# Optimization experiments

Measured on AMD Instinct MI355X. Metric: run time of the kernel, lower is better.

Reference implementation:

```python
import jax, jax.numpy as jnp
import numpy as np

N, E = 50000, 800000
IN, HID, HEADS, EDIM, OUT = 128, 32, 4, 16, 1
W = HID * HEADS  # 128, encoder width


def _glorot(key, shape):
    fan_in = shape[0]
    return jax.random.normal(key, shape, dtype=jnp.float32) / np.sqrt(fan_in)


def setup_inputs() -> dict:
    key = jax.random.key(0)
    ks = jax.random.split(key, 24)
    inp = {
        "x": jax.random.normal(ks[0], (N, IN), dtype=jnp.float32),
        "edge_index": jax.random.randint(ks[1], (2, E), 0, N, dtype=jnp.int64),
        "edge_attr": jax.random.normal(ks[2], (E, EDIM), dtype=jnp.float32),
        # layer 0 (in_channels -> heads*hidden)
        "Wl0": _glorot(ks[3], (IN, W)), "bl0": jnp.zeros((W,), jnp.float32),
        "Wr0": _glorot(ks[4], (IN, W)), "br0": jnp.zeros((W,), jnp.float32),
        "We0": _glorot(ks[5], (EDIM, W)),
        "att0": _glorot(ks[6], (HEADS, HID)),
        "b0": jnp.zeros((W,), jnp.float32),
        # layer 1 (heads*hidden -> heads*hidden)
        "Wl1": _glorot(ks[7], (W, W)), "bl1": jnp.zeros((W,), jnp.float32),
        "Wr1": _glorot(ks[8], (W, W)), "br1": jnp.zeros((W,), jnp.float32),
        "We1": _glorot(ks[9], (EDIM, W)),
        "att1": _glorot(ks[10], (HEADS, HID)),
        "b1": jnp.zeros((W,), jnp.float32),
        # classifier
        "Wc": _glorot(ks[11], (W, OUT)), "bc": jnp.zeros((OUT,), jnp.float32),
    }
    return inp


def _gatv2_layer(x, src, dst, ea, Wl, bl, Wr, br, We, att, b, n_nodes):
    # GATv2Conv (PyG defaults: share_weights=False, negative_slope=0.2, concat=True)
    H, C = att.shape
    xl = (x @ Wl + bl).reshape(n_nodes, H, C)   # source-side transform
    xr = (x @ Wr + br).reshape(n_nodes, H, C)   # target-side transform
    eh = (ea @ We).reshape(-1, H, C)            # edge feature transform (no bias)
    m = xl[src] + xr[dst] + eh                  # [E', H, C] per-edge message pre-activation
    e = jnp.einsum('ehc,hc->eh', jax.nn.leaky_relu(m, 0.2), att)  # [E', H]
    # segment softmax over incoming edges of each dst node (self-loops ensure no empty segment)
    emax = jax.ops.segment_max(e, dst, num_segments=n_nodes)
    ex = jnp.exp(e - emax[dst])
    denom = jax.ops.segment_sum(ex, dst, num_segments=n_nodes)
    alpha = ex / (denom[dst] + 1e-16)
    out = jax.ops.segment_sum(alpha[..., None] * xl[src], dst, num_segments=n_nodes)
    return out.reshape(n_nodes, H * C) + b


def reference(x, edge_index, edge_attr,
              Wl0, bl0, Wr0, br0, We0, att0, b0,
              Wl1, bl1, Wr1, br1, We1, att1, b1,
              Wc, bc):
    n = x.shape[0]
    src, dst = edge_index[0], edge_index[1]
    # add_self_loops with fill_value='mean': self-loop edge_attr = mean of incoming edge_attr per node
    cnt = jax.ops.segment_sum(jnp.ones((src.shape[0],), x.dtype), dst, num_segments=n)
    loop_attr = jax.ops.segment_sum(edge_attr, dst, num_segments=n) / jnp.maximum(cnt, 1.0)[:, None]
    loop = jnp.arange(n, dtype=src.dtype)
    src_a = jnp.concatenate([src, loop])
    dst_a = jnp.concatenate([dst, loop])
    ea_a = jnp.concatenate([edge_attr, loop_attr], axis=0)

    h = jax.nn.gelu(_gatv2_layer(x, src_a, dst_a, ea_a, Wl0, bl0, Wr0, br0, We0, att0, b0, n), approximate=False)
    h = jax.nn.gelu(_gatv2_layer(h, src_a, dst_a, ea_a, Wl1, bl1, Wr1, br1, We1, att1, b1, n), approximate=False)
    logits = h @ Wc + bc  # [N, 1]  (dropout inactive in eval mode)
    return logits.squeeze(-1)
```

## Files before the change

### kernel.cpp

```cpp
#include <hip/hip_runtime.h>
#include <math.h>


static inline size_t align256(size_t x) { return (x + 255) & ~size_t(255); }

__device__ __forceinline__ int clampi(int v, int lo, int hi) {
  return v < lo ? lo : (v > hi ? hi : v);
}

__global__ void k_hist(const int* __restrict__ ei, int* __restrict__ cnt, int E, int n) {
  int i = blockIdx.x * blockDim.x + threadIdx.x;
  if (i >= E) return;
  int dst = clampi(ei[E + i], 0, n - 1);
  atomicAdd(&cnt[dst], 1);
}

__global__ void k_scan(const int* __restrict__ cnt, int* __restrict__ row_ptr, int n) {
  const int T = 1024;
  __shared__ int wsum[16], wbase[16];
  int tid = threadIdx.x;
  int chunk = (n + T - 1) / T;
  int lo = tid * chunk; if (lo > n) lo = n;
  int hi = lo + chunk;  if (hi > n) hi = n;
  int s = 0;
  for (int i = lo; i < hi; ++i) s += cnt[i] + 1;
  int lane = tid & 63, w = tid >> 6;
  int incl = s;
  #pragma unroll
  for (int d = 1; d < 64; d <<= 1) {
    int v = __shfl_up(incl, d, 64);
    if (lane >= d) incl += v;
  }
  if (lane == 63) wsum[w] = incl;
  __syncthreads();
  if (tid == 0) {
    int a = 0;
    for (int i = 0; i < 16; ++i) { wbase[i] = a; a += wsum[i]; }
  }
  __syncthreads();
  int run = wbase[w] + (incl - s);
  if (tid == 0) row_ptr[0] = 0;
  for (int i = lo; i < hi; ++i) { run += cnt[i] + 1; row_ptr[i + 1] = run; }
}

__global__ void k_scatter(const int* __restrict__ ei, int* __restrict__ cursor,
                          int2* __restrict__ col, int E, int n) {
  int i = blockIdx.x * blockDim.x + threadIdx.x;
  if (i < E) {
    int src = clampi(ei[i], 0, n - 1);
    int dst = clampi(ei[E + i], 0, n - 1);
    int pos = atomicAdd(&cursor[dst], 1);
    col[pos] = make_int2(src, i);
  } else if (i < E + n) {
    int node = i - E;
    int pos = atomicAdd(&cursor[node], 1);
    col[pos] = make_int2(node, E + node);
  }
}

__global__ void k_loop_mean(const int* __restrict__ row_ptr, const int2* __restrict__ col,
                            const float* __restrict__ ea, float* __restrict__ lsum,
                            int n, int E) {
  int t = blockIdx.x * blockDim.x + threadIdx.x;
  if (t >= n * 16) return;
  int node = t >> 4, d = t & 15;
  int beg = row_ptr[node], end = row_ptr[node + 1];
  float s = 0.f;
  int c = 0;
  for (int i = beg; i < end; ++i) {
    int2 se = col[i];
    if (se.y < E) { s += ea[(size_t)se.y * 16 + d]; ++c; }
  }
  lsum[t] = s / (float)(c > 0 ? c : 1);
}

__launch_bounds__(256)
__global__ void k_transform(const float* __restrict__ in, const float* __restrict__ Wl,
                            const float* __restrict__ bl, const float* __restrict__ Wr,
                            const float* __restrict__ br, float* __restrict__ xl,
                            float* __restrict__ xr, int n) {
  __shared__ float As[16][128];
  int tid = threadIdx.x;
  int row0 = blockIdx.x * 16;
  int rows = n - row0; if (rows > 16) rows = 16;
  const float4* in4 = (const float4*)(in + (size_t)row0 * 128);
  float4* As4 = (float4*)As;
  for (int i = tid; i < rows * 32; i += 256) As4[i] = in4[i];
  __syncthreads();
  int c = tid;
  const float* B = (c < 128) ? Wl : Wr;
  int cc = c & 127;
  float bias = (c < 128) ? bl[cc] : br[cc];
  float acc[16];
  #pragma unroll
  for (int i = 0; i < 16; ++i) acc[i] = bias;
  for (int k = 0; k < 128; k += 4) {
    float b0 = B[(k + 0) * 128 + cc], b1 = B[(k + 1) * 128 + cc];
    float b2 = B[(k + 2) * 128 + cc], b3 = B[(k + 3) * 128 + cc];
    #pragma unroll
    for (int r = 0; r < 16; ++r) {
      float4 a = *(const float4*)&As[r][k];
      acc[r] += a.x * b0 + a.y * b1 + a.z * b2 + a.w * b3;
    }
  }
  float* op = (c < 128) ? xl : xr;
  for (int r = 0; r < rows; ++r) op[(size_t)(row0 + r) * 128 + cc] = acc[r];
}

#define EDGE_STEP(SRC, EID, MX, DEN, A0, A1)                                     \
  do {                                                                           \
    const float* ep = ((EID) < E) ? (ea + (size_t)(EID) * 16)                    \
                                  : (loop_attr + (size_t)((EID) - E) * 16);      \
    float2 xlv = *(const float2*)(xl + (size_t)(SRC) * 128 + lane * 2);          \
    float4 v0 = ((const float4*)ep)[0];                                          \
    float4 v1 = ((const float4*)ep)[1];                                          \
    float4 v2 = ((const float4*)ep)[2];                                          \
    float4 v3 = ((const float4*)ep)[3];                                          \
    float eh0 = v0.x * we0[0] + v0.y * we0[1] + v0.z * we0[2] + v0.w * we0[3];   \
    float eh1 = v0.x * we1[0] + v0.y * we1[1] + v0.z * we1[2] + v0.w * we1[3];   \
    eh0 += v1.x * we0[4] + v1.y * we0[5] + v1.z * we0[6] + v1.w * we0[7];        \
    eh1 += v1.x * we1[4] + v1.y * we1[5] + v1.z * we1[6] + v1.w * we1[7];        \
    eh0 += v2.x * we0[8] + v2.y * we0[9] + v2.z * we0[10] + v2.w * we0[11];      \
    eh1 += v2.x * we1[8] + v2.y * we1[9] + v2.z * we1[10] + v2.w * we1[11];      \
    eh0 += v3.x * we0[12] + v3.y * we0[13] + v3.z * we0[14] + v3.w * we0[15];    \
    eh1 += v3.x * we1[12] + v3.y * we1[13] + v3.z * we1[14] + v3.w * we1[15];    \
    float m0 = xlv.x + xrv.x + eh0;                                              \
    float m1 = xlv.y + xrv.y + eh1;                                              \
    float l0 = fmaxf(m0, 0.2f * m0);                        \
    float l1 = fmaxf(m1, 0.2f * m1);                                             \
    float p = l0 * att0 + l1 * att1;                                             \
    p += __shfl_xor(p, 1);                                                       \
    p += __shfl_xor(p, 2);                                                       \
    p += __shfl_xor(p, 4);                                                       \
    p += __shfl_xor(p, 8);                                                       \
    float nm = fmaxf(MX, p);                                                     \
    float sc = __expf(MX - nm);                                                  \
    float w  = __expf(p - nm);                                                   \
    DEN = DEN * sc + w;                                                          \
    A0  = A0 * sc + w * xlv.x;                                                   \
    A1  = A1 * sc + w * xlv.y;                                                   \
    MX  = nm;                                                                    \
  } while (0)

__launch_bounds__(256)
__global__ void k_aggregate(const float* __restrict__ xl, const float* __restrict__ xr,
                            const int* __restrict__ row_ptr, const int2* __restrict__ col,
                            const float* __restrict__ ea, const float* __restrict__ loop_attr,
                            const float* __restrict__ We, const float* __restrict__ att,
                            const float* __restrict__ bvec, float* __restrict__ out,
                            int n, int E) {
  int wv = threadIdx.x >> 6, lane = threadIdx.x & 63;
  int node = blockIdx.x * 4 + wv;
  if (node >= n) return;
  int c0 = lane * 2, c1 = lane * 2 + 1;
  float we0[16], we1[16];
  #pragma unroll
  for (int d = 0; d < 16; ++d) {
    we0[d] = We[d * 128 + c0];
    we1[d] = We[d * 128 + c1];
  }
  float att0 = att[c0], att1 = att[c1];
  float2 xrv = *(const float2*)(xr + (size_t)node * 128 + lane * 2);
  int beg = __builtin_amdgcn_readfirstlane(row_ptr[node]);
  int end = __builtin_amdgcn_readfirstlane(row_ptr[node + 1]);
  float mA = -INFINITY, dA = 0.f, a0A = 0.f, a1A = 0.f;
  float mB = -INFINITY, dB = 0.f, a0B = 0.f, a1B = 0.f;
  int i = beg;
  #pragma unroll 2
  for (; i + 1 < end; i += 2) {
    int2 sa = col[i];
    int2 sb = col[i + 1];
    int srcA = __builtin_amdgcn_readfirstlane(sa.x);
    int eidA = __builtin_amdgcn_readfirstlane(sa.y);
    int srcB = __builtin_amdgcn_readfirstlane(sb.x);
    int eidB = __builtin_amdgcn_readfirstlane(sb.y);
    EDGE_STEP(srcA, eidA, mA, dA, a0A, a1A);
    EDGE_STEP(srcB, eidB, mB, dB, a0B, a1B);
  }
  if (i < end) {
    int2 sa = col[i];
    int srcA = __builtin_amdgcn_readfirstlane(sa.x);
    int eidA = __builtin_amdgcn_readfirstlane(sa.y);
    EDGE_STEP(srcA, eidA, mA, dA, a0A, a1A);
  }
  float nm = fmaxf(mA, mB);
  float eA = __expf(mA - nm), eB = __expf(mB - nm);
  float den  = dA * eA + dB * eB;
  float acc0 = a0A * eA + a0B * eB;
  float acc1 = a1A * eA + a1B * eB;
  float inv = 1.f / (den + 1e-16f);
  float2 bv = ((const float2*)bvec)[lane];
  float o0 = acc0 * inv + bv.x;
  float o1 = acc1 * inv + bv.y;
  o0 = 0.5f * o0 * (1.f + erff(o0 * 0.70710678118654752f));
  o1 = 0.5f * o1 * (1.f + erff(o1 * 0.70710678118654752f));
  *(float2*)(out + (size_t)node * 128 + lane * 2) = make_float2(o0, o1);
}

__global__ void k_classifier(const float* __restrict__ h, const float* __restrict__ Wc,
                             const float* __restrict__ bc, float* __restrict__ out, int n) {
  int node = blockIdx.x * blockDim.x + threadIdx.x;
  if (node >= n) return;
  const float4* hp = (const float4*)(h + (size_t)node * 128);
  const float4* wp = (const float4*)Wc;
  float acc = 0.f;
  #pragma unroll
  for (int k = 0; k < 32; ++k) {
    float4 a = hp[k];
    float4 w = wp[k];
    acc += a.x * w.x + a.y * w.y + a.z * w.z + a.w * w.w;
  }
  out[node] = acc + bc[0];
}

extern "C" void kernel_launch(void* const* d_in, const int* in_sizes, int n_in,
                              void* d_out, int out_size, void* d_ws, size_t ws_size,
                              hipStream_t stream) {
  const float* x    = (const float*)d_in[0];
  const int*   ei   = (const int*)d_in[1];
  const float* ea   = (const float*)d_in[2];
  const float* Wl0  = (const float*)d_in[3];
  const float* bl0  = (const float*)d_in[4];
  const float* Wr0  = (const float*)d_in[5];
  const float* br0  = (const float*)d_in[6];
  const float* We0  = (const float*)d_in[7];
  const float* att0 = (const float*)d_in[8];
  const float* b0   = (const float*)d_in[9];
  const float* Wl1  = (const float*)d_in[10];
  const float* bl1  = (const float*)d_in[11];
  const float* Wr1  = (const float*)d_in[12];
  const float* br1  = (const float*)d_in[13];
  const float* We1  = (const float*)d_in[14];
  const float* att1 = (const float*)d_in[15];
  const float* b1   = (const float*)d_in[16];
  const float* Wc   = (const float*)d_in[17];
  const float* bc   = (const float*)d_in[18];
  float* out = (float*)d_out;

  int n  = in_sizes[0] / 128;
  int E  = in_sizes[1] / 2;
  int Ep = E + n;

  char* ws = (char*)d_ws;
  size_t off = 0;
  auto alloc = [&](size_t bytes) { size_t o = off; off = align256(off + bytes); return o; };
  int*   cnt     = (int*)  (ws + alloc((size_t)n * 4));
  float* lsum    = (float*)(ws + alloc((size_t)n * 16 * 4));
  int*   row_ptr = (int*)  (ws + alloc((size_t)(n + 1) * 4));
  int*   cursor  = (int*)  (ws + alloc((size_t)n * 4));
  int2*  col     = (int2*) (ws + alloc((size_t)Ep * 8));
  float* xl      = (float*)(ws + alloc((size_t)n * 128 * 4));
  float* xr      = (float*)(ws + alloc((size_t)n * 128 * 4));
  float* hbuf    = (float*)(ws + alloc((size_t)n * 128 * 4));
  (void)ws_size; (void)n_in; (void)out_size;

  hipMemsetAsync(cnt, 0, (size_t)n * 4, stream);
  k_hist<<<(E + 255) / 256, 256, 0, stream>>>(ei, cnt, E, n);
  k_scan<<<1, 1024, 0, stream>>>(cnt, row_ptr, n);
  hipMemcpyAsync(cursor, row_ptr, (size_t)n * 4, hipMemcpyDeviceToDevice, stream);
  k_scatter<<<(Ep + 255) / 256, 256, 0, stream>>>(ei, cursor, col, E, n);
  k_loop_mean<<<(n * 16 + 255) / 256, 256, 0, stream>>>(row_ptr, col, ea, lsum, n, E);

  k_transform<<<(n + 15) / 16, 256, 0, stream>>>(x, Wl0, bl0, Wr0, br0, xl, xr, n);
  k_aggregate<<<(n + 3) / 4, 256, 0, stream>>>(xl, xr, row_ptr, col, ea, lsum,
                                               We0, att0, b0, hbuf, n, E);
  k_transform<<<(n + 15) / 16, 256, 0, stream>>>(hbuf, Wl1, bl1, Wr1, br1, xl, xr, n);
  k_aggregate<<<(n + 3) / 4, 256, 0, stream>>>(xl, xr, row_ptr, col, ea, lsum,
                                               We1, att1, b1, hbuf, n, E);
  k_classifier<<<(n + 255) / 256, 256, 0, stream>>>(hbuf, Wc, bc, out, n);
}
```

Before: 821.0 us.

## Fuse classifier into final aggregate, widen edge unroll, drop LDS in transform

The final aggregate kernel now computes the classifier dot product with a wave-wide shuffle reduction and writes logits directly. This removes the classifier launch and the write and re-read of the final hidden buffer. The aggregate loop now keeps four independent online-softmax accumulators instead of two, giving more memory-level parallelism across edges. The transform kernel handles 32 rows per block and reads activations straight from global memory (broadcast float4 loads) instead of staging them in LDS, at the cost of more registers and uncached-in-LDS reads.

```diff
diff --git a/kernel.cpp b/kernel.cpp
--- a/kernel.cpp
+++ b/kernel.cpp
@@ -74,36 +74,43 @@
   lsum[t] = s / (float)(c > 0 ? c : 1);
 }
 
+#define TR_ROWS 32
 __launch_bounds__(256)
 __global__ void k_transform(const float* __restrict__ in, const float* __restrict__ Wl,
                             const float* __restrict__ bl, const float* __restrict__ Wr,
                             const float* __restrict__ br, float* __restrict__ xl,
                             float* __restrict__ xr, int n) {
-  __shared__ float As[16][128];
   int tid = threadIdx.x;
-  int row0 = blockIdx.x * 16;
-  int rows = n - row0; if (rows > 16) rows = 16;
-  const float4* in4 = (const float4*)(in + (size_t)row0 * 128);
-  float4* As4 = (float4*)As;
-  for (int i = tid; i < rows * 32; i += 256) As4[i] = in4[i];
-  __syncthreads();
-  int c = tid;
-  const float* B = (c < 128) ? Wl : Wr;
-  int cc = c & 127;
-  float bias = (c < 128) ? bl[cc] : br[cc];
-  float acc[16];
+  int row0 = blockIdx.x * TR_ROWS;
+  int rows = n - row0; if (rows > TR_ROWS) rows = TR_ROWS;
+  int cc = tid & 127;
+  const float* B = (tid < 128) ? Wl : Wr;
+  float bias = (tid < 128) ? bl[cc] : br[cc];
+  float acc[TR_ROWS];
   #pragma unroll
-  for (int i = 0; i < 16; ++i) acc[i] = bias;
-  for (int k = 0; k < 128; k += 4) {
-    float b0 = B[(k + 0) * 128 + cc], b1 = B[(k + 1) * 128 + cc];
-    float b2 = B[(k + 2) * 128 + cc], b3 = B[(k + 3) * 128 + cc];
-    #pragma unroll
-    for (int r = 0; r < 16; ++r) {
-      float4 a = *(const float4*)&As[r][k];
-      acc[r] += a.x * b0 + a.y * b1 + a.z * b2 + a.w * b3;
+  for (int r = 0; r < TR_ROWS; ++r) acc[r] = bias;
+  const float* Ab = in + (size_t)row0 * 128;
+  if (rows == TR_ROWS) {
+    for (int k = 0; k < 128; k += 4) {
+      float b0 = B[(k + 0) * 128 + cc], b1 = B[(k + 1) * 128 + cc];
+      float b2 = B[(k + 2) * 128 + cc], b3 = B[(k + 3) * 128 + cc];
+      #pragma unroll
+      for (int r = 0; r < TR_ROWS; ++r) {
+        float4 a = *(const float4*)(Ab + r * 128 + k);
+        acc[r] += a.x * b0 + a.y * b1 + a.z * b2 + a.w * b3;
+      }
     }
-  }
-  float* op = (c < 128) ? xl : xr;
+  } else {
+    for (int k = 0; k < 128; k += 4) {
+      float b0 = B[(k + 0) * 128 + cc], b1 = B[(k + 1) * 128 + cc];
+      float b2 = B[(k + 2) * 128 + cc], b3 = B[(k + 3) * 128 + cc];
+      for (int r = 0; r < rows; ++r) {
+        float4 a = *(const float4*)(Ab + r * 128 + k);
+        acc[r] += a.x * b0 + a.y * b1 + a.z * b2 + a.w * b3;
+      }
+    }
+  }
+  float* op = (tid < 128) ? xl : xr;
   for (int r = 0; r < rows; ++r) op[(size_t)(row0 + r) * 128 + cc] = acc[r];
 }
 
@@ -147,7 +154,8 @@
                             const int* __restrict__ row_ptr, const int2* __restrict__ col,
                             const float* __restrict__ ea, const float* __restrict__ loop_attr,
                             const float* __restrict__ We, const float* __restrict__ att,
-                            const float* __restrict__ bvec, float* __restrict__ out,
+                            const float* __restrict__ bvec, float* __restrict__ outv,
+                            const float* __restrict__ Wc, const float* __restrict__ bc,
                             int n, int E) {
   int wv = threadIdx.x >> 6, lane = threadIdx.x & 63;
   int node = blockIdx.x * 4 + wv;
@@ -165,52 +173,54 @@
   int end = __builtin_amdgcn_readfirstlane(row_ptr[node + 1]);
   float mA = -INFINITY, dA = 0.f, a0A = 0.f, a1A = 0.f;
   float mB = -INFINITY, dB = 0.f, a0B = 0.f, a1B = 0.f;
+  float mC = -INFINITY, dC = 0.f, a0C = 0.f, a1C = 0.f;
+  float mD = -INFINITY, dD = 0.f, a0D = 0.f, a1D = 0.f;
   int i = beg;
-  #pragma unroll 2
-  for (; i + 1 < end; i += 2) {
-    int2 sa = col[i];
-    int2 sb = col[i + 1];
-    int srcA = __builtin_amdgcn_readfirstlane(sa.x);
-    int eidA = __builtin_amdgcn_readfirstlane(sa.y);
-    int srcB = __builtin_amdgcn_readfirstlane(sb.x);
-    int eidB = __builtin_amdgcn_readfirstlane(sb.y);
+  for (; i + 3 < end; i += 4) {
+    int2 s0 = col[i], s1 = col[i + 1], s2 = col[i + 2], s3 = col[i + 3];
+    int srcA = __builtin_amdgcn_readfirstlane(s0.x);
+    int eidA = __builtin_amdgcn_readfirstlane(s0.y);
+    int srcB = __builtin_amdgcn_readfirstlane(s1.x);
+    int eidB = __builtin_amdgcn_readfirstlane(s1.y);
+    int srcC = __builtin_amdgcn_readfirstlane(s2.x);
+    int eidC = __builtin_amdgcn_readfirstlane(s2.y);
+    int srcD = __builtin_amdgcn_readfirstlane(s3.x);
+    int eidD = __builtin_amdgcn_readfirstlane(s3.y);
     EDGE_STEP(srcA, eidA, mA, dA, a0A, a1A);
     EDGE_STEP(srcB, eidB, mB, dB, a0B, a1B);
-  }
-  if (i < end) {
-    int2 sa = col[i];
-    int srcA = __builtin_amdgcn_readfirstlane(sa.x);
-    int eidA = __builtin_amdgcn_readfirstlane(sa.y);
+    EDGE_STEP(srcC, eidC, mC, dC, a0C, a1C);
+    EDGE_STEP(srcD, eidD, mD, dD, a0D, a1D);
+  }
+  for (; i < end; ++i) {
+    int2 s0 = col[i];
+    int srcA = __builtin_amdgcn_readfirstlane(s0.x);
+    int eidA = __builtin_amdgcn_readfirstlane(s0.y);
     EDGE_STEP(srcA, eidA, mA, dA, a0A, a1A);
   }
-  float nm = fmaxf(mA, mB);
+  float nm = fmaxf(fmaxf(mA, mB), fmaxf(mC, mD));
   float eA = __expf(mA - nm), eB = __expf(mB - nm);
-  float den  = dA * eA + dB * eB;
-  float acc0 = a0A * eA + a0B * eB;
-  float acc1 = a1A * eA + a1B * eB;
+  float eC = __expf(mC - nm), eD = __expf(mD - nm);
+  float den  = dA * eA + dB * eB + dC * eC + dD * eD;
+  float acc0 = a0A * eA + a0B * eB + a0C * eC + a0D * eD;
+  float acc1 = a1A * eA + a1B * eB + a1C * eC + a1D * eD;
   float inv = 1.f / (den + 1e-16f);
   float2 bv = ((const float2*)bvec)[lane];
   float o0 = acc0 * inv + bv.x;
   float o1 = acc1 * inv + bv.y;
   o0 = 0.5f * o0 * (1.f + erff(o0 * 0.70710678118654752f));
   o1 = 0.5f * o1 * (1.f + erff(o1 * 0.70710678118654752f));
-  *(float2*)(out + (size_t)node * 128 + lane * 2) = make_float2(o0, o1);
-}
-
-__global__ void k_classifier(const float* __restrict__ h, const float* __restrict__ Wc,
-                             const float* __restrict__ bc, float* __restrict__ out, int n) {
-  int node = blockIdx.x * blockDim.x + threadIdx.x;
-  if (node >= n) return;
-  const float4* hp = (const float4*)(h + (size_t)node * 128);
-  const float4* wp = (const float4*)Wc;
-  float acc = 0.f;
-  #pragma unroll
-  for (int k = 0; k < 32; ++k) {
-    float4 a = hp[k];
-    float4 w = wp[k];
-    acc += a.x * w.x + a.y * w.y + a.z * w.z + a.w * w.w;
-  }
-  out[node] = acc + bc[0];
+  if (Wc) {
+    float part = o0 * Wc[c0] + o1 * Wc[c1];
+    part += __shfl_xor(part, 1);
+    part += __shfl_xor(part, 2);
+    part += __shfl_xor(part, 4);
+    part += __shfl_xor(part, 8);
+    part += __shfl_xor(part, 16);
+    part += __shfl_xor(part, 32);
+    if (lane == 0) outv[node] = part + bc[0];
+  } else {
+    *(float2*)(outv + (size_t)node * 128 + lane * 2) = make_float2(o0, o1);
+  }
 }
 
 extern "C" void kernel_launch(void* const* d_in, const int* in_sizes, int n_in,
@@ -261,11 +271,10 @@
   k_scatter<<<(Ep + 255) / 256, 256, 0, stream>>>(ei, cursor, col, E, n);
   k_loop_mean<<<(n * 16 + 255) / 256, 256, 0, stream>>>(row_ptr, col, ea, lsum, n, E);
 
-  k_transform<<<(n + 15) / 16, 256, 0, stream>>>(x, Wl0, bl0, Wr0, br0, xl, xr, n);
+  k_transform<<<(n + TR_ROWS - 1) / TR_ROWS, 256, 0, stream>>>(x, Wl0, bl0, Wr0, br0, xl, xr, n);
   k_aggregate<<<(n + 3) / 4, 256, 0, stream>>>(xl, xr, row_ptr, col, ea, lsum,
-                                               We0, att0, b0, hbuf, n, E);
-  k_transform<<<(n + 15) / 16, 256, 0, stream>>>(hbuf, Wl1, bl1, Wr1, br1, xl, xr, n);
+                                               We0, att0, b0, hbuf, nullptr, nullptr, n, E);
+  k_transform<<<(n + TR_ROWS - 1) / TR_ROWS, 256, 0, stream>>>(hbuf, Wl1, bl1, Wr1, br1, xl, xr, n);
   k_aggregate<<<(n + 3) / 4, 256, 0, stream>>>(xl, xr, row_ptr, col, ea, lsum,
-                                               We1, att1, b1, hbuf, n, E);
-  k_classifier<<<(n + 255) / 256, 256, 0, stream>>>(hbuf, Wc, bc, out, n);
-}
+                                               We1, att1, b1, out, Wc, bc, n, E);
+}
```

After: 1.018 ms. 24.0% more time.
